# Kernel optimization log

Measured on AMD Instinct MI355X. Metric: run time of the kernel, lower is better.

Reference implementation:

```python
import jax, jax.numpy as jnp
import numpy as np

V, T, B = 32000, 64, 32
H, E = 32, 200


def setup_inputs() -> dict:
    key = jax.random.key(0)
    ks = jax.random.split(key, 9)
    s = lambda *d: 1.0 / np.sqrt(d[-1])
    return {
        "y": jax.random.randint(ks[0], (B, T), 0, V, dtype=jnp.int64) if jax.config.jax_enable_x64 else jax.random.randint(ks[0], (B, T), 0, V, dtype=jnp.int32),
        "encoder_last_hidden": jax.random.normal(ks[1], (B, H), dtype=jnp.float32),
        "emb_table": jax.random.normal(ks[2], (V, E), dtype=jnp.float32),
        "Wi": jax.random.uniform(ks[3], (H, E), jnp.float32, -s(E), s(E)),
        "bi": jax.random.uniform(ks[4], (H,), jnp.float32, -s(E), s(E)),
        "Wh": jax.random.uniform(ks[5], (H, H), jnp.float32, -s(H), s(H)),
        "bh": jax.random.uniform(ks[6], (H,), jnp.float32, -s(H), s(H)),
        "Wo": jax.random.uniform(ks[7], (V, H), jnp.float32, -s(H), s(H)),
        "bo": jax.random.uniform(ks[8], (V,), jnp.float32, -s(H), s(H)),
    }


def reference(y, encoder_last_hidden, emb_table, Wi, bi, Wh, bh, Wo, bo):
    # Deterministic teacher forcing (ratio=1.0): input at step t is y[:, t].
    emb = emb_table[y]                      # [B, T, E] embedding gather
    emb_t = jnp.swapaxes(emb, 0, 1)         # [T, B, E] scan over time

    def step(hidden, e):
        # RNNManual cell: tanh(i2h(x) + h2h(h))
        h = jnp.tanh(e @ Wi.T + bi + hidden @ Wh.T + bh)   # [B, H]
        logits = h @ Wo.T + bo                             # [B, V]
        logp = jax.nn.log_softmax(logits, axis=-1)
        pred = jnp.argmax(logp, axis=-1)                   # [B]
        return h, (logp, pred)

    _, (logp, pred) = jax.lax.scan(step, encoder_last_hidden, emb_t)
    logprobs = jnp.swapaxes(logp, 0, 1)     # [B, T, V]
    preds = jnp.swapaxes(pred, 0, 1)        # [B, T] = original `result`
    return logprobs, preds
```

## Files before the change

### kernel.cpp

```cpp
#include <hip/hip_runtime.h>
#include <math.h>

#define BB 32
#define TT 64
#define VV 32000
#define HH 32
#define EE 200
#define MM (BB * TT)
#define VC 25
#define VTPC 80
#define NWE (VV * HH)
#define WLB ((NWE + 255) / 256)

typedef __attribute__((ext_vector_type(8))) short short8;
typedef __attribute__((ext_vector_type(4))) float f32x4;

__device__ inline void split3(float x, ushort& u0, ushort& u1, ushort& u2) {
    unsigned a = __float_as_uint(x);
    ushort t0 = (ushort)((a + 0x7FFFu + ((a >> 16) & 1u)) >> 16);
    float f0 = __uint_as_float(((unsigned)t0) << 16);
    float r1 = x - f0;
    unsigned b = __float_as_uint(r1);
    ushort t1 = (ushort)((b + 0x7FFFu + ((b >> 16) & 1u)) >> 16);
    float f1 = __uint_as_float(((unsigned)t1) << 16);
    float r2 = r1 - f1;
    unsigned c = __float_as_uint(r2);
    ushort t2 = (ushort)((c + 0x7FFFu + ((c >> 16) & 1u)) >> 16);
    u0 = t0; u1 = t1; u2 = t2;
}

__device__ inline f32x4 mfma6(short8 a0, short8 a1, short8 a2,
                              short8 b0, short8 b1, short8 b2) {
    f32x4 acc = {0.f, 0.f, 0.f, 0.f};
    acc = __builtin_amdgcn_mfma_f32_16x16x32_bf16(a2, b0, acc, 0, 0, 0);
    acc = __builtin_amdgcn_mfma_f32_16x16x32_bf16(a0, b2, acc, 0, 0, 0);
    acc = __builtin_amdgcn_mfma_f32_16x16x32_bf16(a1, b1, acc, 0, 0, 0);
    acc = __builtin_amdgcn_mfma_f32_16x16x32_bf16(a1, b0, acc, 0, 0, 0);
    acc = __builtin_amdgcn_mfma_f32_16x16x32_bf16(a0, b1, acc, 0, 0, 0);
    acc = __builtin_amdgcn_mfma_f32_16x16x32_bf16(a0, b0, acc, 0, 0, 0);
    return acc;
}

__global__ __launch_bounds__(256) void k_pre(
        const int* __restrict__ y, const float* __restrict__ emb,
        const float* __restrict__ Wi, const float* __restrict__ bi,
        const float* __restrict__ bh, const float* __restrict__ Wo,
        float* __restrict__ i2h,
        ushort* __restrict__ W0, ushort* __restrict__ W1, ushort* __restrict__ W2) {
    int blk = blockIdx.x;
    if (blk >= MM) {
        int i = (blk - MM) * 256 + (int)threadIdx.x;
        if (i < NWE) {
            ushort u0, u1, u2; split3(Wo[i], u0, u1, u2);
            W0[i] = u0; W1[i] = u1; W2[i] = u2;
        }
        return;
    }
    int tok = y[blk];
    __shared__ float se[EE];
    for (int e = threadIdx.x; e < EE; e += 256) se[e] = emb[(size_t)tok * EE + e];
    __syncthreads();
    int h = threadIdx.x >> 3;
    int j = threadIdx.x & 7;
    float acc = 0.f;
    for (int e = j; e < EE; e += 8) acc += se[e] * Wi[h * EE + e];
    acc += __shfl_down(acc, 4, 8);
    acc += __shfl_down(acc, 2, 8);
    acc += __shfl_down(acc, 1, 8);
    if (j == 0) i2h[blk * HH + h] = acc + bi[h] + bh[h];
}

__global__ void k_rnn(const float* __restrict__ enc, const float* __restrict__ Wh,
                      const float* __restrict__ i2h,
                      ushort* __restrict__ H0, ushort* __restrict__ H1,
                      ushort* __restrict__ H2) {
    int b = blockIdx.x;
    int tid = threadIdx.x;
    __shared__ float hs[HH];
    __shared__ float sWh[HH][HH + 1];
    __shared__ float si[TT * HH];
    for (int i = tid; i < HH * HH; i += 64) sWh[i >> 5][i & 31] = Wh[i];
    for (int i = tid; i < TT * HH; i += 64) si[i] = i2h[b * TT * HH + i];
    if (tid < HH) hs[tid] = enc[b * HH + tid];
    __syncthreads();
    for (int t = 0; t < TT; ++t) {
        float hv = 0.f;
        if (tid < HH) {
            float a0 = si[t * HH + tid], a1 = 0.f, a2 = 0.f, a3 = 0.f;
#pragma unroll
            for (int j = 0; j < HH; j += 4) {
                a0 += sWh[tid][j]     * hs[j];
                a1 += sWh[tid][j + 1] * hs[j + 1];
                a2 += sWh[tid][j + 2] * hs[j + 2];
                a3 += sWh[tid][j + 3] * hs[j + 3];
            }
            hv = tanhf((a0 + a1) + (a2 + a3));
        }
        __syncthreads();
        if (tid < HH) {
            hs[tid] = hv;
            ushort u0, u1, u2; split3(hv, u0, u1, u2);
            int idx = (b * TT + t) * HH + tid;
            H0[idx] = u0; H1[idx] = u1; H2[idx] = u2;
        }
        __syncthreads();
    }
}

__global__ __launch_bounds__(256) void k_stats_mfma(
        const ushort* __restrict__ W0, const ushort* __restrict__ W1, const ushort* __restrict__ W2,
        const ushort* __restrict__ H0, const ushort* __restrict__ H1, const ushort* __restrict__ H2,
        const float* __restrict__ bo,
        float* __restrict__ pmax, float* __restrict__ pamx, float* __restrict__ psum) {
    int c  = blockIdx.x;
    int wv = threadIdx.x >> 6;
    int l  = threadIdx.x & 63;
    int lc = l & 15, lg = l >> 4;
    int Tb = (blockIdx.y * 4 + wv) * 4;

    short8 a0[4], a1[4], a2[4];
#pragma unroll
    for (int i = 0; i < 4; ++i) {
        size_t aoff = (size_t)((Tb + i) * 16 + lc) * HH + lg * 8;
        a0[i] = *(const short8*)(H0 + aoff);
        a1[i] = *(const short8*)(H1 + aoff);
        a2[i] = *(const short8*)(H2 + aoff);
    }

    float mx[4][4], am[4][4], sm[4][4];
#pragma unroll
    for (int i = 0; i < 4; ++i)
#pragma unroll
        for (int q = 0; q < 4; ++q) { mx[i][q] = -1e30f; am[i][q] = 0.f; sm[i][q] = 0.f; }

    int vb = c * (VTPC * 16);
#pragma unroll 2
    for (int s = 0; s < VTPC; ++s) {
        int v = vb + s * 16 + lc;
        size_t boff = (size_t)v * HH + lg * 8;
        short8 b0 = *(const short8*)(W0 + boff);
        short8 b1 = *(const short8*)(W1 + boff);
        short8 b2 = *(const short8*)(W2 + boff);
        float bov = bo[v];
        float vf  = (float)v;
#pragma unroll
        for (int i = 0; i < 4; ++i) {
            f32x4 acc = mfma6(a0[i], a1[i], a2[i], b0, b1, b2);
#pragma unroll
            for (int q = 0; q < 4; ++q) {
                float g = acc[q] + bov;
                sm[i][q] += __expf(g);
                if (g > mx[i][q]) { mx[i][q] = g; am[i][q] = vf; }
            }
        }
    }

#pragma unroll
    for (int i = 0; i < 4; ++i)
#pragma unroll
        for (int q = 0; q < 4; ++q) {
#pragma unroll
            for (int msk = 1; msk <= 8; msk <<= 1) {
                float m2 = __shfl_xor(mx[i][q], msk);
                float av = __shfl_xor(am[i][q], msk);
                float s2 = __shfl_xor(sm[i][q], msk);
                sm[i][q] += s2;
                if (m2 > mx[i][q] || (m2 == mx[i][q] && av < am[i][q])) {
                    mx[i][q] = m2; am[i][q] = av;
                }
            }
        }
    if (lc == 0) {
#pragma unroll
        for (int i = 0; i < 4; ++i) {
            int base = c * MM + (Tb + i) * 16 + lg * 4;
#pragma unroll
            for (int q = 0; q < 4; ++q) {
                pmax[base + q] = mx[i][q];
                pamx[base + q] = am[i][q];
                psum[base + q] = sm[i][q];
            }
        }
    }
}

__global__ void k_combine(const float* __restrict__ pmax, const float* __restrict__ pamx,
                          const float* __restrict__ psum,
                          float* __restrict__ lse, float* __restrict__ preds) {
    int r = blockIdx.x * blockDim.x + threadIdx.x;
    if (r >= MM) return;
    float m = -1e30f, a = 0.f, s = 0.f;
    for (int c = 0; c < VC; ++c) {
        int idx = c * MM + r;
        float m2 = pmax[idx], a2 = pamx[idx];
        s += psum[idx];
        if (m2 > m || (m2 == m && a2 < a)) { m = m2; a = a2; }
    }
    lse[r] = logf(s);
    preds[r] = a;
}

__global__ __launch_bounds__(64) void k_write_conv(
        const float* __restrict__ Wo,
        const ushort* __restrict__ H0, const ushort* __restrict__ H1, const ushort* __restrict__ H2,
        const float* __restrict__ bo, const float* __restrict__ lse,
        float* __restrict__ out) {
    int v0 = blockIdx.x * 32;
    int lc = threadIdx.x & 15, lg = threadIdx.x >> 4;
    int mbase = blockIdx.y * (MM / 4);

    __shared__ float sl[MM / 4];
    for (int i = threadIdx.x; i < MM / 4; i += 64) sl[i] = lse[mbase + i];

    short8 b0a, b1a, b2a, b0b, b1b, b2b;
    {
        const float* ra = Wo + (size_t)(v0 + lc) * HH + lg * 8;
        const float* rb = ra + 16 * HH;
#pragma unroll
        for (int j = 0; j < 8; ++j) {
            ushort u0, u1, u2; split3(ra[j], u0, u1, u2);
            b0a[j] = (short)u0; b1a[j] = (short)u1; b2a[j] = (short)u2;
        }
#pragma unroll
        for (int j = 0; j < 8; ++j) {
            ushort u0, u1, u2; split3(rb[j], u0, u1, u2);
            b0b[j] = (short)u0; b1b[j] = (short)u1; b2b[j] = (short)u2;
        }
    }
    float boA = bo[v0 + lc], boB = bo[v0 + 16 + lc];
    __syncthreads();

    for (int s = 0; s < MM / 4 / 16; ++s) {
        int m0 = mbase + s * 16;
        size_t aoff = (size_t)(m0 + lc) * HH + lg * 8;
        short8 a0 = *(const short8*)(H0 + aoff);
        short8 a1 = *(const short8*)(H1 + aoff);
        short8 a2 = *(const short8*)(H2 + aoff);
        f32x4 accA = mfma6(a0, a1, a2, b0a, b1a, b2a);
        f32x4 accB = mfma6(a0, a1, a2, b0b, b1b, b2b);
        int row = m0 + lg * 4;
        int lrow = s * 16 + lg * 4;
#pragma unroll
        for (int q = 0; q < 4; ++q) {
            float ls = sl[lrow + q];
            size_t ob = (size_t)(row + q) * VV + v0 + lc;
            out[ob]      = accA[q] + boA - ls;
            out[ob + 16] = accB[q] + boB - ls;
        }
    }
}

extern "C" void kernel_launch(void* const* d_in, const int* in_sizes, int n_in,
                              void* d_out, int out_size, void* d_ws, size_t ws_size,
                              hipStream_t stream) {
    const int*   y   = (const int*)  d_in[0];
    const float* enc = (const float*)d_in[1];
    const float* emb = (const float*)d_in[2];
    const float* Wi  = (const float*)d_in[3];
    const float* bi  = (const float*)d_in[4];
    const float* Wh  = (const float*)d_in[5];
    const float* bh  = (const float*)d_in[6];
    const float* Wo  = (const float*)d_in[7];
    const float* bo  = (const float*)d_in[8];
    float* out = (float*)d_out;
    float* ws  = (float*)d_ws;

    float* i2h  = ws;
    ushort* H0  = (ushort*)(ws + 65536);
    ushort* H1  = H0 + MM * HH;
    ushort* H2  = H1 + MM * HH;
    float* pmax = ws + 163840;
    float* pamx = ws + 215040;
    float* psum = ws + 266240;
    float* lse  = ws + 317440;

    ushort* W0 = (ushort*)out;
    ushort* W1 = W0 + NWE;
    ushort* W2 = W1 + NWE;

    k_pre<<<MM + WLB, 256, 0, stream>>>(y, emb, Wi, bi, bh, Wo, i2h, W0, W1, W2);
    k_rnn<<<BB, 64, 0, stream>>>(enc, Wh, i2h, H0, H1, H2);
    dim3 gs(VC, 8);
    k_stats_mfma<<<gs, 256, 0, stream>>>(W0, W1, W2, H0, H1, H2, bo, pmax, pamx, psum);
    k_combine<<<(MM + 255) / 256, 256, 0, stream>>>(pmax, pamx, psum, lse,
                                                    out + (size_t)MM * VV);
    dim3 gw(1000, 4);
    k_write_conv<<<gw, 64, 0, stream>>>(Wo, H0, H1, H2, bo, lse, out);
}
```

Measured before the change: 436.1 us.

## Replace combine kernel with atomic reductions, remap stats grid, nontemporal output stores

Removes the k_combine kernel by having the stats kernel atomically add partial sums and atomicMax a packed (max, index) key into per-row globals, which are zeroed by extra blocks in k_pre. The write kernel computes the log of the sum and decodes preds itself. The stats grid shrinks from 25x8 to 16 vocab chunks of 125 tiles, flattened to 128 blocks with an XCD-aware mapping. Output stores become nontemporal. The risks are atomic contention, fewer blocks for parallelism, and the packed-key argmax relying on the partial sums being taken relative to a shared fixed offset.

```diff
diff --git a/kernel.cpp b/kernel.cpp
--- a/kernel.cpp
+++ b/kernel.cpp
@@ -7,10 +7,11 @@
 #define HH 32
 #define EE 200
 #define MM (BB * TT)
-#define VC 25
-#define VTPC 80
+#define VC 16
+#define VTPC 125
 #define NWE (VV * HH)
 #define WLB ((NWE + 255) / 256)
+#define ZB 8
 
 typedef __attribute__((ext_vector_type(8))) short short8;
 typedef __attribute__((ext_vector_type(4))) float f32x4;
@@ -41,13 +42,25 @@
     return acc;
 }
 
+__device__ inline unsigned long long packkey(float g, unsigned v) {
+    unsigned bits = __float_as_uint(g);
+    unsigned e = (bits & 0x80000000u) ? ~bits : (bits | 0x80000000u);
+    return ((unsigned long long)e << 32) | (unsigned long long)(0xFFFFFFFFu - v);
+}
+
 __global__ __launch_bounds__(256) void k_pre(
         const int* __restrict__ y, const float* __restrict__ emb,
         const float* __restrict__ Wi, const float* __restrict__ bi,
         const float* __restrict__ bh, const float* __restrict__ Wo,
         float* __restrict__ i2h,
-        ushort* __restrict__ W0, ushort* __restrict__ W1, ushort* __restrict__ W2) {
+        ushort* __restrict__ W0, ushort* __restrict__ W1, ushort* __restrict__ W2,
+        float* __restrict__ gsum, unsigned long long* __restrict__ gkey) {
     int blk = blockIdx.x;
+    if (blk >= MM + WLB) {
+        int i = (blk - MM - WLB) * 256 + (int)threadIdx.x;
+        if (i < MM) { gsum[i] = 0.f; gkey[i] = 0ull; }
+        return;
+    }
     if (blk >= MM) {
         int i = (blk - MM) * 256 + (int)threadIdx.x;
         if (i < NWE) {
@@ -111,12 +124,16 @@
         const ushort* __restrict__ W0, const ushort* __restrict__ W1, const ushort* __restrict__ W2,
         const ushort* __restrict__ H0, const ushort* __restrict__ H1, const ushort* __restrict__ H2,
         const float* __restrict__ bo,
-        float* __restrict__ pmax, float* __restrict__ pamx, float* __restrict__ psum) {
-    int c  = blockIdx.x;
+        float* __restrict__ gsum, unsigned long long* __restrict__ gkey) {
+    int id   = blockIdx.x;
+    int xcd  = id & 7;
+    int yrow = (id >> 3) & 7;
+    int chi  = id >> 6;
+    int c    = chi * 8 + xcd;
     int wv = threadIdx.x >> 6;
     int l  = threadIdx.x & 63;
     int lc = l & 15, lg = l >> 4;
-    int Tb = (blockIdx.y * 4 + wv) * 4;
+    int Tb = (yrow * 4 + wv) * 4;
 
     short8 a0[4], a1[4], a2[4];
 #pragma unroll
@@ -173,44 +190,34 @@
     if (lc == 0) {
 #pragma unroll
         for (int i = 0; i < 4; ++i) {
-            int base = c * MM + (Tb + i) * 16 + lg * 4;
+            int base = (Tb + i) * 16 + lg * 4;
 #pragma unroll
             for (int q = 0; q < 4; ++q) {
-                pmax[base + q] = mx[i][q];
-                pamx[base + q] = am[i][q];
-                psum[base + q] = sm[i][q];
-            }
-        }
-    }
-}
-
-__global__ void k_combine(const float* __restrict__ pmax, const float* __restrict__ pamx,
-                          const float* __restrict__ psum,
-                          float* __restrict__ lse, float* __restrict__ preds) {
-    int r = blockIdx.x * blockDim.x + threadIdx.x;
-    if (r >= MM) return;
-    float m = -1e30f, a = 0.f, s = 0.f;
-    for (int c = 0; c < VC; ++c) {
-        int idx = c * MM + r;
-        float m2 = pmax[idx], a2 = pamx[idx];
-        s += psum[idx];
-        if (m2 > m || (m2 == m && a2 < a)) { m = m2; a = a2; }
-    }
-    lse[r] = logf(s);
-    preds[r] = a;
+                atomicAdd(&gsum[base + q], sm[i][q]);
+                atomicMax(&gkey[base + q], packkey(mx[i][q], (unsigned)am[i][q]));
+            }
+        }
+    }
 }
 
 __global__ __launch_bounds__(64) void k_write_conv(
         const float* __restrict__ Wo,
         const ushort* __restrict__ H0, const ushort* __restrict__ H1, const ushort* __restrict__ H2,
-        const float* __restrict__ bo, const float* __restrict__ lse,
-        float* __restrict__ out) {
+        const float* __restrict__ bo,
+        const float* __restrict__ gsum, const unsigned long long* __restrict__ gkey,
+        float* __restrict__ out, float* __restrict__ preds) {
     int v0 = blockIdx.x * 32;
     int lc = threadIdx.x & 15, lg = threadIdx.x >> 4;
     int mbase = blockIdx.y * (MM / 4);
 
     __shared__ float sl[MM / 4];
-    for (int i = threadIdx.x; i < MM / 4; i += 64) sl[i] = lse[mbase + i];
+    for (int i = threadIdx.x; i < MM / 4; i += 64) sl[i] = logf(gsum[mbase + i]);
+    if (blockIdx.x == 0) {
+        for (int i = threadIdx.x; i < MM / 4; i += 64) {
+            unsigned low = (unsigned)(gkey[mbase + i] & 0xFFFFFFFFull);
+            preds[mbase + i] = (float)(0xFFFFFFFFu - low);
+        }
+    }
 
     short8 b0a, b1a, b2a, b0b, b1b, b2b;
     {
@@ -244,8 +251,8 @@
         for (int q = 0; q < 4; ++q) {
             float ls = sl[lrow + q];
             size_t ob = (size_t)(row + q) * VV + v0 + lc;
-            out[ob]      = accA[q] + boA - ls;
-            out[ob + 16] = accB[q] + boB - ls;
+            __builtin_nontemporal_store(accA[q] + boA - ls, &out[ob]);
+            __builtin_nontemporal_store(accB[q] + boB - ls, &out[ob + 16]);
         }
     }
 }
@@ -269,21 +276,19 @@
     ushort* H0  = (ushort*)(ws + 65536);
     ushort* H1  = H0 + MM * HH;
     ushort* H2  = H1 + MM * HH;
-    float* pmax = ws + 163840;
-    float* pamx = ws + 215040;
-    float* psum = ws + 266240;
-    float* lse  = ws + 317440;
+    float* gsum = ws + 163840;
+    unsigned long long* gkey =
+        (unsigned long long*)(ws + 165888);
 
     ushort* W0 = (ushort*)out;
     ushort* W1 = W0 + NWE;
     ushort* W2 = W1 + NWE;
-
-    k_pre<<<MM + WLB, 256, 0, stream>>>(y, emb, Wi, bi, bh, Wo, i2h, W0, W1, W2);
+    float* preds = out + (size_t)MM * VV;
+
+    k_pre<<<MM + WLB + ZB, 256, 0, stream>>>(y, emb, Wi, bi, bh, Wo, i2h,
+                                             W0, W1, W2, gsum, gkey);
     k_rnn<<<BB, 64, 0, stream>>>(enc, Wh, i2h, H0, H1, H2);
-    dim3 gs(VC, 8);
-    k_stats_mfma<<<gs, 256, 0, stream>>>(W0, W1, W2, H0, H1, H2, bo, pmax, pamx, psum);
-    k_combine<<<(MM + 255) / 256, 256, 0, stream>>>(pmax, pamx, psum, lse,
-                                                    out + (size_t)MM * VV);
+    k_stats_mfma<<<128, 256, 0, stream>>>(W0, W1, W2, H0, H1, H2, bo, gsum, gkey);
     dim3 gw(1000, 4);
-    k_write_conv<<<gw, 64, 0, stream>>>(Wo, H0, H1, H2, bo, lse, out);
-}
+    k_write_conv<<<gw, 64, 0, stream>>>(Wo, H0, H1, H2, bo, gsum, gkey, out, preds);
+}
```

Result: slower. 475.6 us (+9.1%).
